# Kernel tuning notes

Measured on AMD Instinct MI355X. Metric: run time of the kernel, lower is better.

Reference implementation:

```python
import math
import jax, jax.numpy as jnp
import numpy as np

NPIX = 262144  # 512x512 flattened pixel map


def _shift_matrix(kmax):
    """Faithful numpy port of EPG.EPG_shift_matrices (incl. the S[0:2,4]=1 quirk)."""
    N = 3 * (kmax + 1)
    Sf = np.zeros((N * N,), dtype=np.complex64)
    kidx = list(range(3, N, 3))
    sidx = [x - 3 for x in kidx]
    Sf[[a + N * b for a, b in zip(kidx, sidx)]] = 1
    kidx = list(range(4, N, 3))[:-1]
    sidx = [x + 3 for x in kidx]
    Sf[[a + N * b for a, b in zip(kidx, sidx)]] = 1
    kidx = list(range(2, N, 3))
    Sf[[a + N * a for a in kidx]] = 1
    S = Sf.reshape(N, N).T.copy()
    S[0:2, 4] = 1
    return S


def _rf_rot(alpha, phi):
    """Faithful numpy port of EPG.RF_rot (complex 3x3 RF rotation)."""
    cos2 = np.cos(alpha / 2.0) ** 2
    sin2 = np.sin(alpha / 2.0) ** 2
    sina = np.sin(alpha)
    cosa = np.cos(alpha)
    r10 = np.exp(-2j * phi) * sin2
    RR = np.array([
        [cos2, np.conj(r10), -1j * np.exp(1j * phi) * sina],
        [r10, cos2, 1j * np.exp(-1j * phi) * sina],
        [-0.5j * np.exp(-1j * phi) * sina, 0.5j * np.exp(1j * phi) * sina, cosa],
    ], dtype=np.complex64)
    return RR


def setup_inputs() -> dict:
    key = jax.random.key(0)
    qm = jax.random.uniform(key, (1, 3, NPIX, 1), dtype=jnp.float32)
    return {"quantitative_maps": qm, "n_pulses": 32, "TR": 15}


def reference(quantitative_maps, n_pulses, TR):
    # forward(): PD/T1/T2 maps, each [npix, 1]
    PD = quantitative_maps[0, 0, :, :]
    T1 = quantitative_maps[0, 1, :, :] * 5000.0 + 0.01
    T2 = quantitative_maps[0, 2, :, :] * 1500.0 + 0.01
    TRf = jnp.float32(TR)

    # EPG_GRE static setup (kmax_per_pulse cap logic from the source)
    np2 = int(n_pulses)
    kpp = list(range(1, math.ceil(np2 / 2) + 1)) + list(range(math.floor(np2 / 2), 0, -1))
    kmax = min(np2 - 1, max(kpp))
    K = kmax + 1
    N = 3 * K  # EPG state width (F+, F-, Z per k-order)

    S = jnp.asarray(_shift_matrix(kmax))  # [N, N] complex64, gradient shift
    # theta = 0.25*pi for every pulse (forward hardcodes this) -> A constant
    A = jnp.asarray(_rf_rot(0.25 * np.pi, 0.0))  # [3, 3] complex64

    E1 = jnp.exp(-TRf / T1)[:, 0]  # [npix]
    E2 = jnp.exp(-TRf / T2)[:, 0]  # [npix]
    # E = kron(I_K, diag(E2, E2, E1)) is diagonal -> keep only the diagonal vector
    Evec = jnp.tile(jnp.stack([E2, E2, E1], axis=1), (1, K)).astype(jnp.complex64)  # [npix, N]
    b = jnp.zeros((E1.shape[0], N), jnp.complex64).at[:, 2].set(1.0 - E1)

    FF0 = jnp.zeros((E1.shape[0], N), jnp.complex64).at[:, 2].set(1.0)

    def step(FF, _):
        # T = kron(I_K, A): apply A to each 3-block of the state
        Fj = jnp.einsum('ij,pkj->pki', A, FF.reshape(-1, K, 3)).reshape(FF.shape)  # [npix, N]
        # relaxation + shift + recovery, then conjugation (as in EPG_GRE loop)
        FF_next = jnp.conj(Evec * (Fj @ S.T) + b)
        return FF_next, Fj[:, 0]  # echo = F+0 state after RF pulse

    _, echoes = jax.lax.scan(step, FF0, None, length=np2)  # [np2, npix]
    s = echoes.T  # [npix, np2] == F[:, 0, :]
    return jnp.abs(s) * PD  # PD [npix,1] broadcasts -> [npix, np2]
```

## Files before the change

kernel.cpp:

```cpp
#include <hip/hip_runtime.h>
#include <math.h>
#include <utility>


#define NPULSES 32
#define KK 18
#define KMAX 17

__host__ __device__ constexpr int cmin3(int a, int b, int c) {
    int m = a < b ? a : b; return m < c ? m : c;
}

template <typename F, int... Ts>
__device__ __forceinline__ void static_for(F&& f, std::integer_sequence<int, Ts...>) {
    (f(std::integral_constant<int, Ts>{}), ...);
}

__global__ __launch_bounds__(256) void epg_kernel(
    const float* __restrict__ qm,
    const int* __restrict__ tr_ptr,
    float* __restrict__ out,
    int npix)
{
    int p = blockIdx.x * blockDim.x + threadIdx.x;
    if (p >= npix) return;

    float PD = qm[p];
    float T1 = fmaf(qm[npix + p], 5000.0f, 0.01f);
    float T2 = fmaf(qm[2 * npix + p], 1500.0f, 0.01f);
    float TR = (float)(*tr_ptr);
    float E1 = __expf(-TR / T1);
    float E2 = __expf(-TR / T2);

    const float c2 = 0.8535533905932737f;
    const float s2 = 0.1464466094067263f;
    const float sa = 0.7071067811865476f;

    float Aa = -E2 * c2;
    float Bb = -E2 * s2;
    float C  =  E2 * sa;
    float D  =  E1 * 0.5f * sa;
    float Ez =  E1 * sa;
    float inj = (1.0f - E1) * PD;

    float fp[KK], fm[KK], z[KK];
    #pragma unroll
    for (int k = 0; k < KK; ++k) { fp[k] = 0.0f; fm[k] = 0.0f; z[k] = 0.0f; }
    z[0] = PD;

    float4* o4 = (float4*)(out + (size_t)p * NPULSES);
    float ebuf[4];

    static_for([&](auto tc) {
        constexpr int t = decltype(tc)::value;
        constexpr int A = cmin3(t, KMAX, (NPULSES - 1) - t);

        float e = fmaf(c2, fp[0], fmaf(s2, fm[0], -sa * z[0]));
        ebuf[t & 3] = fabsf(e);
        if constexpr ((t & 3) == 3) {
            o4[t >> 2] = make_float4(ebuf[0], ebuf[1], ebuf[2], ebuf[3]);
        }

        if constexpr (t < NPULSES - 1) {
            constexpr int B = cmin3(t + 1, KMAX, (NPULSES - 2) - t);

            float Rp[A + 2], Rm[A + 2], Zn[A + 2];
            Rm[A + 1] = 0.0f; Zn[A + 1] = 0.0f;
            #pragma unroll
            for (int k = 0; k <= A; ++k) {
                float pk = fp[k], mk = fm[k], zk = z[k];
                float Cz = C * zk;
                Rp[k] = fmaf(Aa, pk, fmaf(Bb, mk,  Cz));
                Rm[k] = fmaf(Bb, pk, fmaf(Aa, mk, -Cz));
                Zn[k] = fmaf(Ez, zk, D * (pk - mk));
            }

            #pragma unroll
            for (int k = B; k >= 1; --k) fp[k] = Rp[k - 1];
            fp[0] = Rm[1];
            #pragma unroll
            for (int k = 0; k <= B; ++k) fm[k] = (k <= A) ? Rm[k + 1] : 0.0f;
            #pragma unroll
            for (int k = 0; k <= B; ++k) z[k] = Zn[k];
            z[0] += inj;
        }
    }, std::make_integer_sequence<int, NPULSES>{});
}

extern "C" void kernel_launch(void* const* d_in, const int* in_sizes, int n_in,
                              void* d_out, int out_size, void* d_ws, size_t ws_size,
                              hipStream_t stream) {
    const float* qm = (const float*)d_in[0];
    const int* tr = (const int*)d_in[2];
    float* out = (float*)d_out;
    int npix = in_sizes[0] / 3;

    int block = 256;
    int grid = (npix + block - 1) / block;
    epg_kernel<<<grid, block, 0, stream>>>(qm, tr, out, npix);
}
```

Baseline: 20.43 us.

## Stage echo outputs in LDS for coalesced stores and update EPG state in place

Each thread now writes its echo magnitudes into a padded shared-memory tile instead of issuing per-thread float4 stores directly to global memory. After a barrier, each wavefront writes its 64 pixels back with lane-contiguous float4 stores, so the global write pattern becomes coalesced. The state recurrence is also rewritten to run in descending k order and overwrite fp/fm/z in place, which removes the temporary Rp/Rm/Zn arrays and shrinks the state arrays to cut register use. The LDS tile costs about 33 KB per block, which may limit occupancy. Partial wavefronts at the tail are not written.

```diff
diff --git a/kernel.cpp b/kernel.cpp
--- a/kernel.cpp
+++ b/kernel.cpp
@@ -4,7 +4,6 @@
 
 
 #define NPULSES 32
-#define KK 18
 #define KMAX 17
 
 __host__ __device__ constexpr int cmin3(int a, int b, int c) {
@@ -22,12 +21,14 @@
     float* __restrict__ out,
     int npix)
 {
-    int p = blockIdx.x * blockDim.x + threadIdx.x;
-    if (p >= npix) return;
+    __shared__ float lds[256 * 33];
+    const int tid = threadIdx.x;
+    const int p = blockIdx.x * 256 + tid;
+    const bool valid = (p < npix);
 
-    float PD = qm[p];
-    float T1 = fmaf(qm[npix + p], 5000.0f, 0.01f);
-    float T2 = fmaf(qm[2 * npix + p], 1500.0f, 0.01f);
+    float PD = valid ? qm[p] : 0.0f;
+    float T1 = valid ? fmaf(qm[npix + p], 5000.0f, 0.01f) : 1.0f;
+    float T2 = valid ? fmaf(qm[2 * npix + p], 1500.0f, 0.01f) : 1.0f;
     float TR = (float)(*tr_ptr);
     float E1 = __expf(-TR / T1);
     float E2 = __expf(-TR / T2);
@@ -43,48 +44,54 @@
     float Ez =  E1 * sa;
     float inj = (1.0f - E1) * PD;
 
-    float fp[KK], fm[KK], z[KK];
+    float fp[KMAX], fm[KMAX - 1], z[KMAX - 1];
     #pragma unroll
-    for (int k = 0; k < KK; ++k) { fp[k] = 0.0f; fm[k] = 0.0f; z[k] = 0.0f; }
+    for (int k = 0; k < KMAX; ++k) fp[k] = 0.0f;
+    #pragma unroll
+    for (int k = 0; k < KMAX - 1; ++k) { fm[k] = 0.0f; z[k] = 0.0f; }
     z[0] = PD;
-
-    float4* o4 = (float4*)(out + (size_t)p * NPULSES);
-    float ebuf[4];
 
     static_for([&](auto tc) {
         constexpr int t = decltype(tc)::value;
         constexpr int A = cmin3(t, KMAX, (NPULSES - 1) - t);
 
         float e = fmaf(c2, fp[0], fmaf(s2, fm[0], -sa * z[0]));
-        ebuf[t & 3] = fabsf(e);
-        if constexpr ((t & 3) == 3) {
-            o4[t >> 2] = make_float4(ebuf[0], ebuf[1], ebuf[2], ebuf[3]);
-        }
+        lds[tid * 33 + t] = fabsf(e);
 
         if constexpr (t < NPULSES - 1) {
-            constexpr int B = cmin3(t + 1, KMAX, (NPULSES - 2) - t);
-
-            float Rp[A + 2], Rm[A + 2], Zn[A + 2];
-            Rm[A + 1] = 0.0f; Zn[A + 1] = 0.0f;
-            #pragma unroll
-            for (int k = 0; k <= A; ++k) {
-                float pk = fp[k], mk = fm[k], zk = z[k];
+            float rm_prev = 0.0f;
+            static_for([&](auto jc) {
+                constexpr int j = A - decltype(jc)::value;
+                float pk = fp[j], mk = fm[j], zk = z[j];
                 float Cz = C * zk;
-                Rp[k] = fmaf(Aa, pk, fmaf(Bb, mk,  Cz));
-                Rm[k] = fmaf(Bb, pk, fmaf(Aa, mk, -Cz));
-                Zn[k] = fmaf(Ez, zk, D * (pk - mk));
-            }
-
-            #pragma unroll
-            for (int k = B; k >= 1; --k) fp[k] = Rp[k - 1];
-            fp[0] = Rm[1];
-            #pragma unroll
-            for (int k = 0; k <= B; ++k) fm[k] = (k <= A) ? Rm[k + 1] : 0.0f;
-            #pragma unroll
-            for (int k = 0; k <= B; ++k) z[k] = Zn[k];
+                float rp = fmaf(Aa, pk, fmaf(Bb, mk,  Cz));
+                float rm = fmaf(Bb, pk, fmaf(Aa, mk, -Cz));
+                float zn = fmaf(Ez, zk, D * (pk - mk));
+                fp[j + 1] = rp;
+                fm[j] = rm_prev;
+                z[j] = zn;
+                rm_prev = rm;
+            }, std::make_integer_sequence<int, A + 1>{});
+            fp[0] = fm[0];
             z[0] += inj;
         }
     }, std::make_integer_sequence<int, NPULSES>{});
+
+    __syncthreads();
+
+    const int l = tid & 63;
+    const int w = tid >> 6;
+    float4* dst = (float4*)(out + ((size_t)blockIdx.x * 256 + w * 64) * NPULSES);
+    const int wave_pix_base = blockIdx.x * 256 + w * 64;
+    if (wave_pix_base + 64 <= npix) {
+        #pragma unroll
+        for (int i = 0; i < 8; ++i) {
+            int q  = i * 8 + (l >> 3);
+            int t0 = (l & 7) * 4;
+            const float* s = &lds[(w * 64 + q) * 33 + t0];
+            dst[i * 64 + l] = make_float4(s[0], s[1], s[2], s[3]);
+        }
+    }
 }
 
 extern "C" void kernel_launch(void* const* d_in, const int* in_sizes, int n_in,
```

Result: slower. 21.13 us (+3.4%).

## Update EPG state in place and roll middle pulses into a fixed-band loop

Applied to the files above, without the earlier changes.

The per-pulse update now writes the shifted F+/F−/Z state back into the same register arrays, instead of staging it through temporary Rp/Rm/Zn arrays. The state arrays shrink to 16 slots. The first 16 pulses stay fully unrolled with growing band widths. The middle 12 pulses run in a rolled loop of 3 iterations, each doing 4 steps at the maximum band width, and the tail steps are unrolled by hand. This aims to cut register pressure and instruction-cache footprint. The cost is extra arithmetic on the middle pulses, which now compute the full band instead of the shrinking one the original used.

```diff
diff --git a/kernel.cpp b/kernel.cpp
--- a/kernel.cpp
+++ b/kernel.cpp
@@ -4,12 +4,7 @@
 
 
 #define NPULSES 32
-#define KK 18
-#define KMAX 17
-
-__host__ __device__ constexpr int cmin3(int a, int b, int c) {
-    int m = a < b ? a : b; return m < c ? m : c;
-}
+#define NSLOT 16
 
 template <typename F, int... Ts>
 __device__ __forceinline__ void static_for(F&& f, std::integer_sequence<int, Ts...>) {
@@ -22,7 +17,7 @@
     float* __restrict__ out,
     int npix)
 {
-    int p = blockIdx.x * blockDim.x + threadIdx.x;
+    const int p = blockIdx.x * 256 + threadIdx.x;
     if (p >= npix) return;
 
     float PD = qm[p];
@@ -38,53 +33,81 @@
 
     float Aa = -E2 * c2;
     float Bb = -E2 * s2;
-    float C  =  E2 * sa;
-    float D  =  E1 * 0.5f * sa;
+    float Cc =  E2 * sa;
+    float Dd =  E1 * 0.5f * sa;
     float Ez =  E1 * sa;
     float inj = (1.0f - E1) * PD;
 
-    float fp[KK], fm[KK], z[KK];
+    float fp[NSLOT], fm[NSLOT], z[NSLOT];
     #pragma unroll
-    for (int k = 0; k < KK; ++k) { fp[k] = 0.0f; fm[k] = 0.0f; z[k] = 0.0f; }
+    for (int k = 0; k < NSLOT; ++k) { fp[k] = 0.0f; fm[k] = 0.0f; z[k] = 0.0f; }
     z[0] = PD;
 
     float4* o4 = (float4*)(out + (size_t)p * NPULSES);
     float ebuf[4];
 
+    auto echo = [&](auto sc) {
+        constexpr int s = decltype(sc)::value;
+        float e = fmaf(c2, fp[0], fmaf(s2, fm[0], -sa * z[0]));
+        ebuf[s] = fabsf(e);
+    };
+
+    auto step_band = [&](auto Ac) {
+        constexpr int A = decltype(Ac)::value;
+        float rm_prev = 0.0f;
+        static_for([&](auto jc) {
+            constexpr int j = A - decltype(jc)::value;
+            float pk = fp[j], zk = z[j];
+            float Cz = Cc * zk;
+            if constexpr (j == NSLOT - 1) {
+                float rm = fmaf(Bb, pk, -Cz);
+                z[j]  = fmaf(Ez, zk, Dd * pk);
+                fm[j] = rm_prev;
+                rm_prev = rm;
+            } else {
+                float mk = fm[j];
+                float rp = fmaf(Aa, pk, fmaf(Bb, mk, Cz));
+                float zn = fmaf(Ez, zk, Dd * (pk - mk));
+                if constexpr (j > 0) {
+                    float rm = fmaf(Bb, pk, fmaf(Aa, mk, -Cz));
+                    fp[j + 1] = rp; fm[j] = rm_prev; z[j] = zn;
+                    rm_prev = rm;
+                } else {
+                    fp[1] = rp; fm[0] = rm_prev; z[0] = zn;
+                }
+            }
+        }, std::make_integer_sequence<int, A + 1>{});
+        fp[0] = fm[0];
+        z[0] += inj;
+    };
+
     static_for([&](auto tc) {
         constexpr int t = decltype(tc)::value;
-        constexpr int A = cmin3(t, KMAX, (NPULSES - 1) - t);
+        echo(std::integral_constant<int, t & 3>{});
+        step_band(std::integral_constant<int, t>{});
+        if constexpr ((t & 3) == 3)
+            o4[t >> 2] = make_float4(ebuf[0], ebuf[1], ebuf[2], ebuf[3]);
+    }, std::make_integer_sequence<int, 16>{});
 
-        float e = fmaf(c2, fp[0], fmaf(s2, fm[0], -sa * z[0]));
-        ebuf[t & 3] = fabsf(e);
-        if constexpr ((t & 3) == 3) {
-            o4[t >> 2] = make_float4(ebuf[0], ebuf[1], ebuf[2], ebuf[3]);
-        }
+    float4* optr = o4 + 4;
+    #pragma unroll 1
+    for (int it = 0; it < 3; ++it) {
+        static_for([&](auto sc) {
+            echo(sc);
+            step_band(std::integral_constant<int, NSLOT - 1>{});
+        }, std::make_integer_sequence<int, 4>{});
+        *optr = make_float4(ebuf[0], ebuf[1], ebuf[2], ebuf[3]);
+        ++optr;
+    }
 
-        if constexpr (t < NPULSES - 1) {
-            constexpr int B = cmin3(t + 1, KMAX, (NPULSES - 2) - t);
-
-            float Rp[A + 2], Rm[A + 2], Zn[A + 2];
-            Rm[A + 1] = 0.0f; Zn[A + 1] = 0.0f;
-            #pragma unroll
-            for (int k = 0; k <= A; ++k) {
-                float pk = fp[k], mk = fm[k], zk = z[k];
-                float Cz = C * zk;
-                Rp[k] = fmaf(Aa, pk, fmaf(Bb, mk,  Cz));
-                Rm[k] = fmaf(Bb, pk, fmaf(Aa, mk, -Cz));
-                Zn[k] = fmaf(Ez, zk, D * (pk - mk));
-            }
-
-            #pragma unroll
-            for (int k = B; k >= 1; --k) fp[k] = Rp[k - 1];
-            fp[0] = Rm[1];
-            #pragma unroll
-            for (int k = 0; k <= B; ++k) fm[k] = (k <= A) ? Rm[k + 1] : 0.0f;
-            #pragma unroll
-            for (int k = 0; k <= B; ++k) z[k] = Zn[k];
-            z[0] += inj;
-        }
-    }, std::make_integer_sequence<int, NPULSES>{});
+    echo(std::integral_constant<int, 0>{});
+    step_band(std::integral_constant<int, 3>{});
+    echo(std::integral_constant<int, 1>{});
+    step_band(std::integral_constant<int, 2>{});
+    echo(std::integral_constant<int, 2>{});
+    step_band(std::integral_constant<int, 1>{});
+    echo(std::integral_constant<int, 3>{});
+    o4[7] = make_float4(ebuf[0], ebuf[1], ebuf[2], ebuf[3]);
 }
 
 extern "C" void kernel_launch(void* const* d_in, const int* in_sizes, int n_in,
```

Result: slower. 26.69 us (+30.6%).
